# Optimization experiments

Measured on AMD Instinct MI355X. Metric: run time of the kernel, lower is better.

## Reference

```python
import jax, jax.numpy as jnp
import numpy as np

N_BOXES, N_VIEWS, C_FEAT, HF, WF = 256, 6, 256, 116, 200
IMG_H, IMG_W = 928, 1600
EPS = 1e-8


def setup_inputs() -> dict:
    key = jax.random.key(0)
    k1, k2, k3 = jax.random.split(key, 3)
    # Boxes: centers in front of the cameras so many (box, view) pairs are valid.
    xy = jax.random.uniform(k1, (N_BOXES, 2), minval=-8.0, maxval=8.0)
    z = jax.random.uniform(k2, (N_BOXES, 1), minval=1.0, maxval=40.0)
    rest = jax.random.normal(k3, (N_BOXES, 4)) * 0.5 + 2.0  # l, w, h, heading (unused by loss)
    pred_boxes_3d = jnp.concatenate([xy[:, :1], xy[:, 1:2], z, rest], axis=1).astype(jnp.float32)
    feats = jax.random.normal(jax.random.fold_in(key, 1), (N_VIEWS, C_FEAT, HF, WF), dtype=jnp.float32)
    # Intrinsics: fx=fy=1000, cx=800, cy=464; third row [0,0,1].
    K_one = jnp.array([[1000.0, 0.0, 800.0], [0.0, 1000.0, 464.0], [0.0, 0.0, 1.0]], dtype=jnp.float32)
    K = jnp.broadcast_to(K_one, (N_VIEWS, 3, 3))
    # Extrinsics: identity camera poses (camera at origin looking +z).
    T = jnp.broadcast_to(jnp.eye(4, dtype=jnp.float32), (N_VIEWS, 4, 4))
    img_sizes = jnp.broadcast_to(jnp.array([IMG_H, IMG_W], dtype=jnp.int32), (N_VIEWS, 2))
    return {"pred_boxes_3d": pred_boxes_3d, "feats": feats, "K": K, "T": T, "img_sizes": img_sizes}


def reference(pred_boxes_3d, feats, K, T, img_sizes):
    N = pred_boxes_3d.shape[0]
    V, C, Hf, Wf = feats.shape
    centers = pred_boxes_3d[:, :3]                                   # (N, 3)
    R, t = T[:, :3, :3], T[:, :3, 3]
    p_cam = jnp.einsum('vij,nj->nvi', R, centers) + t[None]          # (N, V, 3)
    p_2d = jnp.einsum('vij,nvj->nvi', K, p_cam)                      # (N, V, 3)
    z = p_cam[..., 2]
    u = p_2d[..., 0] / p_2d[..., 2]
    v = p_2d[..., 1] / z                                             # quirk: divides by point_cam z
    Wimg = img_sizes[:, 1].astype(jnp.float32)[None, :]              # (1, V)
    Himg = img_sizes[:, 0].astype(jnp.float32)[None, :]
    u_s = u * Wf / Wimg
    v_s = v * Hf / Himg
    u0 = jnp.floor(u_s).astype(jnp.int32)                            # u >= 0 on valid pairs -> floor == int()
    v0 = jnp.floor(v_s).astype(jnp.int32)
    valid = ((z > 0) & (u >= 0) & (u < Wimg) & (v >= 0) & (v < Himg)
             & (u0 < Wf - 1) & (v0 < Hf - 1))                        # (N, V)
    u0c = jnp.clip(u0, 0, Wf - 2)
    v0c = jnp.clip(v0, 0, Hf - 2)
    view = jnp.broadcast_to(jnp.arange(V)[None, :], (N, V))
    # mean of the 2x2 feature patch -> (N, V, C)
    fm = (feats[view, :, v0c, u0c] + feats[view, :, v0c, u0c + 1]
          + feats[view, :, v0c + 1, u0c] + feats[view, :, v0c + 1, u0c + 1]) * 0.25
    P = N * V
    fm_f = fm.reshape(P, C)
    valid_f = valid.reshape(P)
    # first valid pair in (box-major, view-minor) order is the stored anchor feature
    first = jnp.argmax(valid_f)
    stored = fm_f[first]                                             # (C,)
    cos = (fm_f @ stored) / (jnp.maximum(jnp.linalg.norm(fm_f, axis=1), EPS)
                             * jnp.maximum(jnp.linalg.norm(stored), EPS))
    loss_i = 1.0 - cos                                               # cosine_embedding_loss, target=1
    mask = valid_f & (jnp.arange(P) != first)                        # anchor pair itself contributes nothing
    n_pairs = jnp.sum(mask)
    total = jnp.sum(jnp.where(mask, loss_i, 0.0))
    return jnp.where(n_pairs > 0, total / jnp.maximum(n_pairs, 1).astype(total.dtype), jnp.zeros((), total.dtype))
```

## Files before the change

### kernel.cpp

```cpp
#include <hip/hip_runtime.h>
#include <math.h>

#define N_BOXES 256
#define N_VIEWS 6
#define C_FEAT 256
#define HF 116
#define WF 200
#define FEAT_HW (HF * WF)
#define P_TOT (N_BOXES * N_VIEWS)
#define EPS_F 1e-8f

struct WsLayout {
    int   count;
    int   pad[15];
    float loss[P_TOT];
};

__device__ __forceinline__ float wave_reduce_sum(float v) {
    #pragma unroll
    for (int off = 32; off > 0; off >>= 1)
        v += __shfl_down(v, off, 64);
    return v;
}

__device__ __forceinline__ int project_pack(
    const float* __restrict__ boxes, const float* __restrict__ Km,
    const float* __restrict__ Tm, const int* __restrict__ img, int p)
{
    const int n = p / N_VIEWS, v = p - n * N_VIEWS;
    const float cx = boxes[n * 7 + 0];
    const float cy = boxes[n * 7 + 1];
    const float cz = boxes[n * 7 + 2];
    const float* Tv = Tm + v * 16;
    const float* Kv = Km + v * 9;
    float pc[3];
    #pragma unroll
    for (int i = 0; i < 3; ++i)
        pc[i] = Tv[i * 4 + 0] * cx + Tv[i * 4 + 1] * cy + Tv[i * 4 + 2] * cz + Tv[i * 4 + 3];
    float p2[3];
    #pragma unroll
    for (int i = 0; i < 3; ++i)
        p2[i] = Kv[i * 3 + 0] * pc[0] + Kv[i * 3 + 1] * pc[1] + Kv[i * 3 + 2] * pc[2];
    const float z  = pc[2];
    const float uu = p2[0] / p2[2];
    const float vv = p2[1] / z;
    const float Wimg = (float)img[v * 2 + 1];
    const float Himg = (float)img[v * 2 + 0];
    const int u0 = (int)floorf(uu * (float)WF / Wimg);
    const int v0 = (int)floorf(vv * (float)HF / Himg);
    const bool valid = (z > 0.f) && (uu >= 0.f) && (uu < Wimg) &&
                       (vv >= 0.f) && (vv < Himg) &&
                       (u0 < WF - 1) && (v0 < HF - 1);
    const int u0c = min(max(u0, 0), WF - 2);
    const int v0c = min(max(v0, 0), HF - 2);
    return u0c | (v0c << 9) | (valid ? (int)0x80000000 : 0);
}

__global__ __launch_bounds__(256) void fused_kernel(
    const float* __restrict__ boxes,
    const float* __restrict__ feats,
    const float* __restrict__ Km,
    const float* __restrict__ Tm,
    const int*   __restrict__ img,
    WsLayout*    __restrict__ ws)
{
    const int tid  = threadIdx.x;
    const int lane = tid & 63;
    const int wave = tid >> 6;

    __shared__ int   s_min[4], s_cnt[4];
    __shared__ float s_fmf[C_FEAT];
    __shared__ float s_red[4];

    const int p = blockIdx.x * 4 + wave;
    const int pk_p = project_pack(boxes, Km, Tm, img, p);
    const bool pvalid = (pk_p < 0);
    float r0[4], r1[4], r2[4], r3[4];
    if (pvalid) {
        const int xp = pk_p & 0x1ff, yp = (pk_p >> 9) & 0x7f;
        const int vp = p % N_VIEWS;
        const float* basep = feats + ((size_t)(vp * C_FEAT) * HF + yp) * WF + xp;
        #pragma unroll
        for (int j = 0; j < 4; ++j) {
            const float* bp = basep + (size_t)(lane + 64 * j) * FEAT_HW;
            r0[j] = bp[0];
            r1[j] = bp[1];
            r2[j] = bp[WF];
            r3[j] = bp[WF + 1];
        }
    }

    int localmin = 0x7fffffff;
    int localcnt = 0;
    #pragma unroll
    for (int i = 0; i < P_TOT / 256; ++i) {
        const int q  = tid + 256 * i;
        const int pk = project_pack(boxes, Km, Tm, img, q);
        if (pk < 0) { ++localcnt; if (q < localmin) localmin = q; }
    }
    #pragma unroll
    for (int off = 32; off > 0; off >>= 1) {
        localmin = min(localmin, __shfl_down(localmin, off, 64));
        localcnt += __shfl_down(localcnt, off, 64);
    }
    if (lane == 0) { s_min[wave] = localmin; s_cnt[wave] = localcnt; }
    __syncthreads();
    const int gmin = min(min(s_min[0], s_min[1]), min(s_min[2], s_min[3]));
    const int gcnt = s_cnt[0] + s_cnt[1] + s_cnt[2] + s_cnt[3];
    const bool any_valid = (gmin != 0x7fffffff);
    const int first = any_valid ? gmin : 0;

    if (blockIdx.x == 0 && tid == 0)
        ws->count = gcnt - (any_valid ? 1 : 0);

    const int pk_f = project_pack(boxes, Km, Tm, img, first);
    const int xf = pk_f & 0x1ff, yf = (pk_f >> 9) & 0x7f;
    const int vf = first % N_VIEWS;
    const float* bf = feats + (((size_t)(vf * C_FEAT) + tid) * HF + yf) * WF + xf;
    const float fmf = 0.25f * (bf[0] + bf[1] + bf[WF] + bf[WF + 1]);
    s_fmf[tid] = fmf;
    const float sn = wave_reduce_sum(fmf * fmf);
    if (lane == 0) s_red[wave] = sn;
    __syncthreads();
    const float snsq = s_red[0] + s_red[1] + s_red[2] + s_red[3];

    const bool active = pvalid && (p != first);
    float dot = 0.f, nsq = 0.f;
    if (active) {
        #pragma unroll
        for (int j = 0; j < 4; ++j) {
            const float fmp = 0.25f * (r0[j] + r1[j] + r2[j] + r3[j]);
            dot += fmp * s_fmf[lane + 64 * j];
            nsq += fmp * fmp;
        }
    }
    dot = wave_reduce_sum(dot);
    nsq = wave_reduce_sum(nsq);

    if (lane == 0) {
        float l = 0.f;
        if (active)
            l = 1.0f - dot / (fmaxf(sqrtf(nsq), EPS_F) * fmaxf(sqrtf(snsq), EPS_F));
        ws->loss[p] = l;
    }
}

__global__ __launch_bounds__(256) void finish_kernel(
    const WsLayout* __restrict__ ws,
    float*          __restrict__ out)
{
    __shared__ float s_red[4];
    const int tid = threadIdx.x;
    float s = 0.f;
    #pragma unroll
    for (int i = 0; i < P_TOT / 256; ++i) s += ws->loss[tid + 256 * i];
    s = wave_reduce_sum(s);
    const int lane = tid & 63, wave = tid >> 6;
    if (lane == 0) s_red[wave] = s;
    __syncthreads();
    if (tid == 0) {
        const float total = s_red[0] + s_red[1] + s_red[2] + s_red[3];
        const int   cnt   = ws->count;
        out[0] = (cnt > 0) ? total / (float)cnt : 0.0f;
    }
}

extern "C" void kernel_launch(void* const* d_in, const int* in_sizes, int n_in,
                              void* d_out, int out_size, void* d_ws, size_t ws_size,
                              hipStream_t stream) {
    const float* boxes = (const float*)d_in[0];
    const float* feats = (const float*)d_in[1];
    const float* Km    = (const float*)d_in[2];
    const float* Tm    = (const float*)d_in[3];
    const int*   img   = (const int*)d_in[4];
    float* out = (float*)d_out;
    WsLayout* ws = (WsLayout*)d_ws;

    hipLaunchKernelGGL(fused_kernel, dim3(P_TOT / 4), dim3(256), 0, stream,
                       boxes, feats, Km, Tm, img, ws);
    hipLaunchKernelGGL(finish_kernel, dim3(1), dim3(256), 0, stream,
                       ws, out);
}
```

Baseline: 202.4 us.

## Hoist anchor search into single-block kernel and reduce loss with atomic ticket

The search for the first valid pair and the anchor feature gather move out of every block into a one-block preceding kernel, which stores the anchor feature, its squared norm, the first index and the count in workspace. The loss kernel reads these values and sums block losses through a float atomicAdd, and the last block, found by a ticket counter, writes the mean, so the separate finish kernel goes away. This removes redundant per-block projection of all 1536 pairs and one launch, but puts a serial single-block kernel on the critical path and makes the float summation order nondeterministic.

```diff
diff --git a/kernel.cpp b/kernel.cpp
--- a/kernel.cpp
+++ b/kernel.cpp
@@ -9,11 +9,16 @@
 #define FEAT_HW (HF * WF)
 #define P_TOT (N_BOXES * N_VIEWS)
 #define EPS_F 1e-8f
+#define NBLK_B (P_TOT / 4)
 
 struct WsLayout {
-    int   count;
-    int   pad[15];
-    float loss[P_TOT];
+    int      first;
+    int      count;
+    float    snsq;
+    float    total;
+    unsigned ticket;
+    int      pad[11];
+    float    fm[C_FEAT];
 };
 
 __device__ __forceinline__ float wave_reduce_sum(float v) {
@@ -56,7 +61,7 @@
     return u0c | (v0c << 9) | (valid ? (int)0x80000000 : 0);
 }
 
-__global__ __launch_bounds__(256) void fused_kernel(
+__global__ __launch_bounds__(256) void argmax_kernel(
     const float* __restrict__ boxes,
     const float* __restrict__ feats,
     const float* __restrict__ Km,
@@ -69,8 +74,62 @@
     const int wave = tid >> 6;
 
     __shared__ int   s_min[4], s_cnt[4];
+    __shared__ float s_red[4];
+
+    int localmin = 0x7fffffff;
+    int localcnt = 0;
+    #pragma unroll
+    for (int i = 0; i < P_TOT / 256; ++i) {
+        const int q  = tid + 256 * i;
+        const int pk = project_pack(boxes, Km, Tm, img, q);
+        if (pk < 0) { ++localcnt; if (q < localmin) localmin = q; }
+    }
+    #pragma unroll
+    for (int off = 32; off > 0; off >>= 1) {
+        localmin = min(localmin, __shfl_down(localmin, off, 64));
+        localcnt += __shfl_down(localcnt, off, 64);
+    }
+    if (lane == 0) { s_min[wave] = localmin; s_cnt[wave] = localcnt; }
+    __syncthreads();
+    const int gmin = min(min(s_min[0], s_min[1]), min(s_min[2], s_min[3]));
+    const int gcnt = s_cnt[0] + s_cnt[1] + s_cnt[2] + s_cnt[3];
+    const bool any_valid = (gmin != 0x7fffffff);
+    const int first = any_valid ? gmin : 0;
+
+    const int pk_f = project_pack(boxes, Km, Tm, img, first);
+    const int xf = pk_f & 0x1ff, yf = (pk_f >> 9) & 0x7f;
+    const int vf = first % N_VIEWS;
+    const float* bf = feats + (((size_t)(vf * C_FEAT) + tid) * HF + yf) * WF + xf;
+    const float fmf = 0.25f * (bf[0] + bf[1] + bf[WF] + bf[WF + 1]);
+    ws->fm[tid] = fmf;
+
+    const float sn = wave_reduce_sum(fmf * fmf);
+    if (lane == 0) s_red[wave] = sn;
+    __syncthreads();
+    if (tid == 0) {
+        ws->first  = first;
+        ws->count  = gcnt - (any_valid ? 1 : 0);
+        ws->snsq   = s_red[0] + s_red[1] + s_red[2] + s_red[3];
+        ws->total  = 0.0f;
+        ws->ticket = 0u;
+    }
+}
+
+__global__ __launch_bounds__(256) void loss_kernel(
+    const float* __restrict__ boxes,
+    const float* __restrict__ feats,
+    const float* __restrict__ Km,
+    const float* __restrict__ Tm,
+    const int*   __restrict__ img,
+    WsLayout*    __restrict__ ws,
+    float*       __restrict__ out)
+{
+    const int tid  = threadIdx.x;
+    const int lane = tid & 63;
+    const int wave = tid >> 6;
+
     __shared__ float s_fmf[C_FEAT];
-    __shared__ float s_red[4];
+    __shared__ float s_loss[4];
 
     const int p = blockIdx.x * 4 + wave;
     const int pk_p = project_pack(boxes, Km, Tm, img, p);
@@ -90,39 +149,11 @@
         }
     }
 
-    int localmin = 0x7fffffff;
-    int localcnt = 0;
-    #pragma unroll
-    for (int i = 0; i < P_TOT / 256; ++i) {
-        const int q  = tid + 256 * i;
-        const int pk = project_pack(boxes, Km, Tm, img, q);
-        if (pk < 0) { ++localcnt; if (q < localmin) localmin = q; }
-    }
-    #pragma unroll
-    for (int off = 32; off > 0; off >>= 1) {
-        localmin = min(localmin, __shfl_down(localmin, off, 64));
-        localcnt += __shfl_down(localcnt, off, 64);
-    }
-    if (lane == 0) { s_min[wave] = localmin; s_cnt[wave] = localcnt; }
-    __syncthreads();
-    const int gmin = min(min(s_min[0], s_min[1]), min(s_min[2], s_min[3]));
-    const int gcnt = s_cnt[0] + s_cnt[1] + s_cnt[2] + s_cnt[3];
-    const bool any_valid = (gmin != 0x7fffffff);
-    const int first = any_valid ? gmin : 0;
-
-    if (blockIdx.x == 0 && tid == 0)
-        ws->count = gcnt - (any_valid ? 1 : 0);
-
-    const int pk_f = project_pack(boxes, Km, Tm, img, first);
-    const int xf = pk_f & 0x1ff, yf = (pk_f >> 9) & 0x7f;
-    const int vf = first % N_VIEWS;
-    const float* bf = feats + (((size_t)(vf * C_FEAT) + tid) * HF + yf) * WF + xf;
-    const float fmf = 0.25f * (bf[0] + bf[1] + bf[WF] + bf[WF + 1]);
-    s_fmf[tid] = fmf;
-    const float sn = wave_reduce_sum(fmf * fmf);
-    if (lane == 0) s_red[wave] = sn;
-    __syncthreads();
-    const float snsq = s_red[0] + s_red[1] + s_red[2] + s_red[3];
+    s_fmf[tid] = ws->fm[tid];
+    const int   first = ws->first;
+    const int   cnt   = ws->count;
+    const float snsq  = ws->snsq;
+    __syncthreads();
 
     const bool active = pvalid && (p != first);
     float dot = 0.f, nsq = 0.f;
@@ -136,32 +167,26 @@
     }
     dot = wave_reduce_sum(dot);
     nsq = wave_reduce_sum(nsq);
-
     if (lane == 0) {
         float l = 0.f;
         if (active)
             l = 1.0f - dot / (fmaxf(sqrtf(nsq), EPS_F) * fmaxf(sqrtf(snsq), EPS_F));
-        ws->loss[p] = l;
-    }
-}
-
-__global__ __launch_bounds__(256) void finish_kernel(
-    const WsLayout* __restrict__ ws,
-    float*          __restrict__ out)
-{
-    __shared__ float s_red[4];
-    const int tid = threadIdx.x;
-    float s = 0.f;
-    #pragma unroll
-    for (int i = 0; i < P_TOT / 256; ++i) s += ws->loss[tid + 256 * i];
-    s = wave_reduce_sum(s);
-    const int lane = tid & 63, wave = tid >> 6;
-    if (lane == 0) s_red[wave] = s;
-    __syncthreads();
+        s_loss[wave] = l;
+    }
+    __syncthreads();
+
     if (tid == 0) {
-        const float total = s_red[0] + s_red[1] + s_red[2] + s_red[3];
-        const int   cnt   = ws->count;
-        out[0] = (cnt > 0) ? total / (float)cnt : 0.0f;
+        const float blockTotal = s_loss[0] + s_loss[1] + s_loss[2] + s_loss[3];
+        if (blockTotal != 0.f)
+            atomicAdd(&ws->total, blockTotal);
+        __threadfence();
+        const unsigned old = atomicAdd(&ws->ticket, 1u);
+        if (old == (unsigned)(NBLK_B - 1)) {
+            __threadfence();
+            const float tot = __hip_atomic_load(&ws->total, __ATOMIC_RELAXED,
+                                                __HIP_MEMORY_SCOPE_AGENT);
+            out[0] = (cnt > 0) ? tot / (float)cnt : 0.0f;
+        }
     }
 }
 
@@ -176,8 +201,8 @@
     float* out = (float*)d_out;
     WsLayout* ws = (WsLayout*)d_ws;
 
-    hipLaunchKernelGGL(fused_kernel, dim3(P_TOT / 4), dim3(256), 0, stream,
+    hipLaunchKernelGGL(argmax_kernel, dim3(1), dim3(256), 0, stream,
                        boxes, feats, Km, Tm, img, ws);
-    hipLaunchKernelGGL(finish_kernel, dim3(1), dim3(256), 0, stream,
-                       ws, out);
-}
+    hipLaunchKernelGGL(loss_kernel, dim3(NBLK_B), dim3(256), 0, stream,
+                       boxes, feats, Km, Tm, img, ws, out);
+}
```

Result: slower. 222.9 us (+10.2%).
